# Performance work log

Hardware: AMD Instinct MI355X
Metric: run time of the kernel (lower is better)

## Reference

```python
import jax, jax.numpy as jnp
from jax import lax
import numpy as np

B, N, C, M = 4, 20000, 512, 1024  # batch, points, seed_feat_dim, M_POINT
GRASPNESS_THRESHOLD = 0.1


def setup_inputs() -> dict:
    key = jax.random.key(0)
    k1, k2, k3, k4 = jax.random.split(key, 4)
    return {
        "point_clouds": jax.random.uniform(k1, (B, N, 3), jnp.float32),
        "seed_features": jax.random.normal(k2, (B, C, N), jnp.float32),
        "objectness_score": jax.random.normal(k3, (B, 2, N), jnp.float32),
        "graspness_score": jax.random.normal(k4, (B, N), jnp.float32),
    }


def _fps(xyz, mask, m):
    """Furthest point sampling restricted to masked-valid points.
    xyz: (n,3), mask: (n,) bool. Returns (m,) int indices.
    Matches compacted-array FPS: first pick = first valid point."""
    n = xyz.shape[0]
    first = jnp.argmax(mask)
    mind0 = jnp.full((n,), jnp.inf, xyz.dtype)

    def step(carry, _):
        mind, last = carry
        d = jnp.sum((xyz - xyz[last]) ** 2, axis=-1)
        mind = jnp.minimum(mind, d)
        nxt = jnp.argmax(jnp.where(mask, mind, -jnp.inf))
        return (mind, nxt), last

    _, idx = lax.scan(step, (mind0, first), None, length=m)
    return idx


def reference(point_clouds, seed_features, objectness_score, graspness_score):
    # graspable mask: objectness argmax == 1 AND graspness > threshold
    obj_mask = jnp.argmax(objectness_score, axis=1) == 1            # (B,N)
    grasp_mask = graspness_score > GRASPNESS_THRESHOLD              # (B,N)
    mask = obj_mask & grasp_mask

    # masked FPS per batch element (original loops over B)
    fps_idx = jax.vmap(_fps, in_axes=(0, 0, None))(point_clouds, mask, M)  # (B,M)
    xyz_g = jnp.take_along_axis(point_clouds, fps_idx[:, :, None], axis=1)  # (B,M,3)

    # three_nn: 3 nearest neighbors of each sampled point in the full cloud
    d2 = jnp.sum((xyz_g[:, :, None, :] - point_clouds[:, None, :, :]) ** 2, axis=-1)  # (B,M,N)
    neg_d2, idx3 = lax.top_k(-d2, 3)                                # (B,M,3)
    dist = jnp.sqrt(jnp.maximum(-neg_d2, 0.0))
    w = 1.0 / (dist + 1e-8)
    w = w / jnp.sum(w, axis=-1, keepdims=True)                      # (B,M,3)

    # three_interpolate: inverse-distance-weighted gather of features
    feats_n = seed_features.transpose(0, 2, 1)                      # (B,N,C)
    nb = jax.vmap(lambda f, i: f[i])(feats_n, idx3)                 # (B,M,3,C)
    interp = jnp.einsum("bmkc,bmk->bcm", nb, w)                   # (B,C,M)
    return interp
```

## Files before the change

### kernel.cpp

```cpp
#include <hip/hip_runtime.h>
#include <cstdint>

#define BB 4
#define NN 20000
#define CC 512
#define MM 1024
#define GTHR 0.1f
#define FPS_T 512
#define LDSCAP 5120
#define QB 8

#define INFF __builtin_huge_valf()

__global__ __launch_bounds__(1024) void compact_kernel(
    const float* __restrict__ pc, const float* __restrict__ obj,
    const float* __restrict__ grasp, float4* __restrict__ cxyz,
    int* __restrict__ nv) {
  const int b = blockIdx.x;
  const int t = threadIdx.x;
  const int lane = t & 63, w = t >> 6;
  __shared__ int wtot[16];
  const float* pcb = pc + (size_t)b * NN * 3;
  const float* o0 = obj + (size_t)b * 2 * NN;
  const float* o1 = o0 + NN;
  const float* gb = grasp + (size_t)b * NN;
  float4* cxyzb = cxyz + (size_t)b * NN;

  const int SPAN = 1250;
  const int wstart = w * SPAN;

  unsigned vmask = 0;
  int cnt = 0;
#pragma unroll
  for (int g = 0; g < 20; ++g) {
    int off = g * 64 + lane;
    bool v = false;
    if (off < SPAN) {
      int i = wstart + off;
      float a0 = o0[i], a1 = o1[i], gg = gb[i];
      v = (a1 > a0) && (gg > GTHR);
    }
    unsigned long long bal = __ballot(v);
    if (v) vmask |= (1u << g);
    cnt += (int)__popcll(bal);
  }
  if (lane == 0) wtot[w] = cnt;
  __syncthreads();
  int base = 0;
#pragma unroll
  for (int k = 0; k < 16; ++k)
    if (k < w) base += wtot[k];
#pragma unroll
  for (int g = 0; g < 20; ++g) {
    int off = g * 64 + lane;
    bool v = (vmask >> g) & 1u;
    unsigned long long bal = __ballot(v);
    if (v) {
      int i = wstart + off;
      int pos = base + (int)__popcll(bal & ((1ull << lane) - 1ull));
      cxyzb[pos] = make_float4(pcb[3 * i], pcb[3 * i + 1], pcb[3 * i + 2], 0.f);
    }
    base += (int)__popcll(bal);
  }
  if (t == 0) {
    int tot = 0;
#pragma unroll
    for (int k = 0; k < 16; ++k) tot += wtot[k];
    nv[b] = tot;
  }
}

template <int K>
__device__ void fps_lds(int nv_, const float4* __restrict__ cxyzb,
                        float4* __restrict__ fpsXyzb,
                        float* lx, float* ly, float* lz,
                        unsigned long long (*pk)[8]) {
  const int t = threadIdx.x;
  const int lane = t & 63, w = t >> 6;
  float x[K], y[K], z[K], mind[K];
#pragma unroll
  for (int s = 0; s < K; ++s) {
    int j = s * FPS_T + t;
    if (j < nv_) {
      float4 p = cxyzb[j];
      x[s] = p.x; y[s] = p.y; z[s] = p.z; mind[s] = INFF;
      lx[j] = p.x; ly[j] = p.y; lz[j] = p.z;
    } else {
      x[s] = 0.f; y[s] = 0.f; z[s] = 0.f; mind[s] = 0.f;
    }
  }
  __syncthreads();
  float qx = lx[0], qy = ly[0], qz = lz[0];
  if (t == 0) fpsXyzb[0] = make_float4(qx, qy, qz, 0.f);
  int buf = 0;
  for (int r = 1; r < MM; ++r) {
    float bm = -1.f;
    int bs = 0;
#pragma unroll
    for (int s = 0; s < K; ++s) {
      float dx = x[s] - qx, dy = y[s] - qy, dz = z[s] - qz;
      float d = fmaf(dz, dz, fmaf(dy, dy, dx * dx));
      float m = fminf(mind[s], d);
      mind[s] = m;
      bool better = m > bm;
      bm = better ? m : bm;
      bs = better ? s : bs;
    }
    unsigned j = (unsigned)(bs * FPS_T + t);
    unsigned long long key =
        ((unsigned long long)__float_as_uint(bm) << 32) | (unsigned)(~j);
#pragma unroll
    for (int off = 32; off; off >>= 1) {
      unsigned long long ok = __shfl_xor(key, off);
      key = ok > key ? ok : key;
    }
    if (lane == 0) pk[buf][w] = key;
    __syncthreads();
    unsigned long long k0 = pk[buf][lane & 7];
    unsigned long long k1 = __shfl_xor(k0, 1); k0 = k1 > k0 ? k1 : k0;
    k1 = __shfl_xor(k0, 2); k0 = k1 > k0 ? k1 : k0;
    k1 = __shfl_xor(k0, 4); k0 = k1 > k0 ? k1 : k0;
    unsigned jw = ~(unsigned)(k0 & 0xffffffffull);
    qx = lx[jw]; qy = ly[jw]; qz = lz[jw];
    if (t == 0) fpsXyzb[r] = make_float4(qx, qy, qz, 0.f);
    buf ^= 1;
  }
}

__device__ void fps_fallback(int nv_, const float4* __restrict__ cxyzb,
                             float4* __restrict__ fpsXyzb,
                             float* __restrict__ mindg,
                             unsigned long long (*pk)[8]) {
  const int t = threadIdx.x;
  const int lane = t & 63, w = t >> 6;
  for (int j = t; j < nv_; j += FPS_T) mindg[j] = INFF;
  __syncthreads();
  float4 q = cxyzb[0];
  float qx = q.x, qy = q.y, qz = q.z;
  if (t == 0) fpsXyzb[0] = make_float4(qx, qy, qz, 0.f);
  int buf = 0;
  for (int r = 1; r < MM; ++r) {
    float bm = -1.f;
    int bj = 0x7fffffff;
    for (int j = t; j < nv_; j += FPS_T) {
      float4 p = cxyzb[j];
      float dx = p.x - qx, dy = p.y - qy, dz = p.z - qz;
      float d = fmaf(dz, dz, fmaf(dy, dy, dx * dx));
      float m = fminf(mindg[j], d);
      mindg[j] = m;
      bool better = m > bm;
      bm = better ? m : bm;
      bj = better ? j : bj;
    }
    unsigned long long key =
        ((unsigned long long)__float_as_uint(bm) << 32) | (unsigned)(~bj);
#pragma unroll
    for (int off = 32; off; off >>= 1) {
      unsigned long long ok = __shfl_xor(key, off);
      key = ok > key ? ok : key;
    }
    if (lane == 0) pk[buf][w] = key;
    __syncthreads();
    unsigned long long k0 = pk[buf][lane & 7];
    unsigned long long k1 = __shfl_xor(k0, 1); k0 = k1 > k0 ? k1 : k0;
    k1 = __shfl_xor(k0, 2); k0 = k1 > k0 ? k1 : k0;
    k1 = __shfl_xor(k0, 4); k0 = k1 > k0 ? k1 : k0;
    unsigned jw = ~(unsigned)(k0 & 0xffffffffull);
    float4 qq = cxyzb[jw];
    qx = qq.x; qy = qq.y; qz = qq.z;
    if (t == 0) fpsXyzb[r] = make_float4(qx, qy, qz, 0.f);
    buf ^= 1;
  }
}

__global__ __launch_bounds__(FPS_T) void fps_kernel(
    const float* __restrict__ pc, const float4* __restrict__ cxyz,
    const int* __restrict__ nv, float4* __restrict__ fpsXyz,
    float* __restrict__ mindg) {
  __shared__ float lx[LDSCAP], ly[LDSCAP], lz[LDSCAP];
  __shared__ unsigned long long pk[2][8];
  int b = blockIdx.x;
  int nv_ = nv[b];
  const float4* cxyzb = cxyz + (size_t)b * NN;
  float4* fpsXyzb = fpsXyz + (size_t)b * MM;
  if (nv_ == 0) {
    int t = threadIdx.x;
    const float* pcb = pc + (size_t)b * NN * 3;
    float4 p0 = make_float4(pcb[0], pcb[1], pcb[2], 0.f);
    for (int r = t; r < MM; r += FPS_T) fpsXyzb[r] = p0;
    return;
  }
  int slots = (nv_ + FPS_T - 1) / FPS_T;
  if (slots <= 3)       fps_lds<3>(nv_, cxyzb, fpsXyzb, lx, ly, lz, pk);
  else if (slots <= 6)  fps_lds<6>(nv_, cxyzb, fpsXyzb, lx, ly, lz, pk);
  else if (slots <= 9)  fps_lds<9>(nv_, cxyzb, fpsXyzb, lx, ly, lz, pk);
  else if (slots <= 10) fps_lds<10>(nv_, cxyzb, fpsXyzb, lx, ly, lz, pk);
  else fps_fallback(nv_, cxyzb, fpsXyzb, mindg + (size_t)b * NN, pk);
}

__device__ __forceinline__ bool nn_before(float ad, int ai, float bd, int bi) {
  return (ad < bd) || (ad == bd && ai < bi);
}

__device__ __forceinline__ void merge3(float* ad, int* ai,
                                       float b0, float b1, float b2,
                                       int j0, int j1, int j2) {
  bool c0 = nn_before(ad[0], ai[0], b0, j0);
  float r0d = c0 ? ad[0] : b0; int r0i = c0 ? ai[0] : j0;
  float Xd = c0 ? b0 : ad[0];  int Xi = c0 ? j0 : ai[0];
  bool c1 = nn_before(ad[1], ai[1], b1, j1);
  float Yd = c1 ? ad[1] : b1;  int Yi = c1 ? ai[1] : j1;
  bool c2 = nn_before(Xd, Xi, Yd, Yi);
  float r1d = c2 ? Xd : Yd;    int r1i = c2 ? Xi : Yi;
  float Wd = c2 ? Yd : Xd;     int Wi = c2 ? Yi : Xi;
  bool c3 = nn_before(ad[2], ai[2], b2, j2);
  float Vd = c3 ? ad[2] : b2;  int Vi = c3 ? ai[2] : j2;
  bool c4 = nn_before(Wd, Wi, Vd, Vi);
  float r2d = c4 ? Wd : Vd;    int r2i = c4 ? Wi : Vi;
  ad[0] = r0d; ad[1] = r1d; ad[2] = r2d;
  ai[0] = r0i; ai[1] = r1i; ai[2] = r2i;
}

__global__ void three_nn_kernel(const float* __restrict__ pc,
                                const float4* __restrict__ fpsXyz,
                                int* __restrict__ idx3,
                                float* __restrict__ w3) {
  const int blk = blockIdx.x;
  const int b = blk / (MM / QB);
  const int qbase = (blk % (MM / QB)) * QB;
  const int t = threadIdx.x;
  const int lane = t & 63, w = t >> 6;
  const float* pcb = pc + (size_t)b * NN * 3;
  float qx[QB], qy[QB], qz[QB];
#pragma unroll
  for (int qq = 0; qq < QB; ++qq) {
    float4 p = fpsXyz[(size_t)b * MM + qbase + qq];
    qx[qq] = p.x; qy[qq] = p.y; qz[qq] = p.z;
  }
  float qd[QB][3]; int qi[QB][3];
#pragma unroll
  for (int qq = 0; qq < QB; ++qq)
#pragma unroll
    for (int k = 0; k < 3; ++k) { qd[qq][k] = INFF; qi[qq][k] = 0x7fffffff; }

  const int nchunk = (NN + 255) / 256;
  for (int c = 0; c < nchunk; ++c) {
    int i = c * 256 + t;
    if (i < NN) {
      float pxx = pcb[3 * i], pyy = pcb[3 * i + 1], pzz = pcb[3 * i + 2];
#pragma unroll
      for (int qq = 0; qq < QB; ++qq) {
        float dx = pxx - qx[qq], dy = pyy - qy[qq], dz = pzz - qz[qq];
        float d = fmaf(dz, dz, fmaf(dy, dy, dx * dx));
        if (d < qd[qq][2]) {
          bool lt0 = d < qd[qq][0], lt1 = d < qd[qq][1];
          qd[qq][2] = lt1 ? qd[qq][1] : d;  qi[qq][2] = lt1 ? qi[qq][1] : i;
          float nd1 = lt0 ? qd[qq][0] : (lt1 ? d : qd[qq][1]);
          int   ni1 = lt0 ? qi[qq][0] : (lt1 ? i : qi[qq][1]);
          qd[qq][1] = nd1; qi[qq][1] = ni1;
          qd[qq][0] = lt0 ? d : qd[qq][0];  qi[qq][0] = lt0 ? i : qi[qq][0];
        }
      }
    }
  }
#pragma unroll
  for (int off = 32; off; off >>= 1) {
#pragma unroll
    for (int qq = 0; qq < QB; ++qq) {
      float bd0 = __shfl_xor(qd[qq][0], off);
      float bd1 = __shfl_xor(qd[qq][1], off);
      float bd2 = __shfl_xor(qd[qq][2], off);
      int bi0 = __shfl_xor(qi[qq][0], off);
      int bi1 = __shfl_xor(qi[qq][1], off);
      int bi2 = __shfl_xor(qi[qq][2], off);
      merge3(qd[qq], qi[qq], bd0, bd1, bd2, bi0, bi1, bi2);
    }
  }
  __shared__ float smd[4][QB][3];
  __shared__ int smi[4][QB][3];
  if (lane == 0) {
#pragma unroll
    for (int qq = 0; qq < QB; ++qq)
#pragma unroll
      for (int k = 0; k < 3; ++k) { smd[w][qq][k] = qd[qq][k]; smi[w][qq][k] = qi[qq][k]; }
  }
  __syncthreads();
  if (t < QB) {
    int qq = t;
    float fd[3]; int fi[3];
#pragma unroll
    for (int k = 0; k < 3; ++k) { fd[k] = smd[0][qq][k]; fi[k] = smi[0][qq][k]; }
#pragma unroll
    for (int ww = 1; ww < 4; ++ww)
      merge3(fd, fi, smd[ww][qq][0], smd[ww][qq][1], smd[ww][qq][2],
             smi[ww][qq][0], smi[ww][qq][1], smi[ww][qq][2]);
    float wa = 1.f / (sqrtf(fmaxf(fd[0], 0.f)) + 1e-8f);
    float wb = 1.f / (sqrtf(fmaxf(fd[1], 0.f)) + 1e-8f);
    float wc = 1.f / (sqrtf(fmaxf(fd[2], 0.f)) + 1e-8f);
    float s = wa + wb + wc;
    size_t base3 = ((size_t)b * MM + qbase + qq) * 3;
    w3[base3] = wa / s; w3[base3 + 1] = wb / s; w3[base3 + 2] = wc / s;
    idx3[base3] = fi[0]; idx3[base3 + 1] = fi[1]; idx3[base3 + 2] = fi[2];
  }
}

__global__ void interp_kernel(const float* __restrict__ seed,
                              const int* __restrict__ idx3,
                              const float* __restrict__ w3,
                              float* __restrict__ out) {
  const int blk = blockIdx.x;
  const int b = blk / CC;
  const int c = blk % CC;
  const float* row = seed + ((size_t)b * CC + c) * NN;
  const int t = threadIdx.x;
#pragma unroll
  for (int u = 0; u < MM / 256; ++u) {
    int m = u * 256 + t;
    size_t base3 = ((size_t)b * MM + m) * 3;
    int i0 = idx3[base3], i1 = idx3[base3 + 1], i2 = idx3[base3 + 2];
    float w0 = w3[base3], w1 = w3[base3 + 1], w2 = w3[base3 + 2];
    float v = fmaf(w2, row[i2], fmaf(w1, row[i1], w0 * row[i0]));
    out[((size_t)b * CC + c) * MM + m] = v;
  }
}

extern "C" void kernel_launch(void* const* d_in, const int* in_sizes, int n_in,
                              void* d_out, int out_size, void* d_ws,
                              size_t ws_size, hipStream_t stream) {
  (void)in_sizes; (void)n_in; (void)out_size; (void)ws_size;
  const float* pc = (const float*)d_in[0];
  const float* seed = (const float*)d_in[1];
  const float* obj = (const float*)d_in[2];
  const float* grasp = (const float*)d_in[3];
  float* out = (float*)d_out;

  char* p = (char*)d_ws;
  float4* cxyz = (float4*)p;   p += sizeof(float4) * BB * NN;
  float4* fpsXyz = (float4*)p; p += sizeof(float4) * BB * MM;
  int* idx3 = (int*)p;         p += sizeof(int) * BB * MM * 3;
  float* w3 = (float*)p;       p += sizeof(float) * BB * MM * 3;
  float* mindg = (float*)p;    p += sizeof(float) * BB * NN;
  int* nv = (int*)p;           p += sizeof(int) * BB;

  hipLaunchKernelGGL(compact_kernel, dim3(BB), dim3(1024), 0, stream,
                     pc, obj, grasp, cxyz, nv);
  hipLaunchKernelGGL(fps_kernel, dim3(BB), dim3(FPS_T), 0, stream,
                     pc, cxyz, nv, fpsXyz, mindg);
  hipLaunchKernelGGL(three_nn_kernel, dim3(BB * MM / QB), dim3(256), 0, stream,
                     pc, fpsXyz, idx3, w3);
  hipLaunchKernelGGL(interp_kernel, dim3(BB * CC), dim3(256), 0, stream,
                     seed, idx3, w3, out);
}
```

Measured before the change: 1.133 ms.

## Fuse mask compaction into FPS kernel and use value-only wave max with ballot index

Merges the separate compaction kernel into the FPS kernel: each block computes the graspable mask, prefix-sums per wave, and writes compacted xyz straight into LDS, going through global memory only when the count exceeds LDS capacity. This removes one launch and a global round trip. The per-iteration argmax now reduces only the float distance with DPP/swizzle, then recovers the index with a ballot over matching slots, and the cross-wave merge reads packed keys with vector LDS loads. The tie-breaking and zero-mind padding lanes could change which index is chosen in edge cases.

```diff
diff --git a/kernel.cpp b/kernel.cpp
--- a/kernel.cpp
+++ b/kernel.cpp
@@ -11,70 +11,43 @@
 #define QB 8
 
 #define INFF __builtin_huge_valf()
-
-__global__ __launch_bounds__(1024) void compact_kernel(
-    const float* __restrict__ pc, const float* __restrict__ obj,
-    const float* __restrict__ grasp, float4* __restrict__ cxyz,
-    int* __restrict__ nv) {
-  const int b = blockIdx.x;
-  const int t = threadIdx.x;
-  const int lane = t & 63, w = t >> 6;
-  __shared__ int wtot[16];
-  const float* pcb = pc + (size_t)b * NN * 3;
-  const float* o0 = obj + (size_t)b * 2 * NN;
-  const float* o1 = o0 + NN;
-  const float* gb = grasp + (size_t)b * NN;
-  float4* cxyzb = cxyz + (size_t)b * NN;
-
-  const int SPAN = 1250;
-  const int wstart = w * SPAN;
-
-  unsigned vmask = 0;
-  int cnt = 0;
-#pragma unroll
-  for (int g = 0; g < 20; ++g) {
-    int off = g * 64 + lane;
-    bool v = false;
-    if (off < SPAN) {
-      int i = wstart + off;
-      float a0 = o0[i], a1 = o1[i], gg = gb[i];
-      v = (a1 > a0) && (gg > GTHR);
-    }
-    unsigned long long bal = __ballot(v);
-    if (v) vmask |= (1u << g);
-    cnt += (int)__popcll(bal);
-  }
-  if (lane == 0) wtot[w] = cnt;
-  __syncthreads();
-  int base = 0;
-#pragma unroll
-  for (int k = 0; k < 16; ++k)
-    if (k < w) base += wtot[k];
-#pragma unroll
-  for (int g = 0; g < 20; ++g) {
-    int off = g * 64 + lane;
-    bool v = (vmask >> g) & 1u;
-    unsigned long long bal = __ballot(v);
-    if (v) {
-      int i = wstart + off;
-      int pos = base + (int)__popcll(bal & ((1ull << lane) - 1ull));
-      cxyzb[pos] = make_float4(pcb[3 * i], pcb[3 * i + 1], pcb[3 * i + 2], 0.f);
-    }
-    base += (int)__popcll(bal);
-  }
-  if (t == 0) {
-    int tot = 0;
-#pragma unroll
-    for (int k = 0; k < 16; ++k) tot += wtot[k];
-    nv[b] = tot;
-  }
+typedef unsigned long long u64;
+
+__device__ __forceinline__ float wave_max_f32(float v) {
+  int i = __float_as_int(v);
+  i = __builtin_amdgcn_update_dpp(i, i, 0x121, 0xF, 0xF, false);
+  v = fmaxf(v, __int_as_float(i));
+  i = __float_as_int(v);
+  i = __builtin_amdgcn_update_dpp(i, i, 0x122, 0xF, 0xF, false);
+  v = fmaxf(v, __int_as_float(i));
+  i = __float_as_int(v);
+  i = __builtin_amdgcn_update_dpp(i, i, 0x124, 0xF, 0xF, false);
+  v = fmaxf(v, __int_as_float(i));
+  i = __float_as_int(v);
+  i = __builtin_amdgcn_update_dpp(i, i, 0x128, 0xF, 0xF, false);
+  v = fmaxf(v, __int_as_float(i));
+  v = fmaxf(v, __int_as_float(
+                   __builtin_amdgcn_ds_swizzle(__float_as_int(v), 0x401F)));
+  v = fmaxf(v, __shfl_xor(v, 32));
+  return v;
+}
+
+__device__ __forceinline__ unsigned merge8(const u64* pkrow) {
+  const ulonglong2* p2 = (const ulonglong2*)pkrow;
+  ulonglong2 e0 = p2[0], e1 = p2[1], e2 = p2[2], e3 = p2[3];
+  u64 a = e0.x > e0.y ? e0.x : e0.y;
+  u64 b = e1.x > e1.y ? e1.x : e1.y;
+  u64 c = e2.x > e2.y ? e2.x : e2.y;
+  u64 d = e3.x > e3.y ? e3.x : e3.y;
+  a = a > b ? a : b;
+  c = c > d ? c : d;
+  a = a > c ? a : c;
+  return ~(unsigned)(a & 0xffffffffull);
 }
 
 template <int K>
-__device__ void fps_lds(int nv_, const float4* __restrict__ cxyzb,
-                        float4* __restrict__ fpsXyzb,
-                        float* lx, float* ly, float* lz,
-                        unsigned long long (*pk)[8]) {
+__device__ void fps_lds(int nv_, const float2* lxy, const float* lz,
+                        float4* fpsXyzb, u64 (*pk)[8]) {
   const int t = threadIdx.x;
   const int lane = t & 63, w = t >> 6;
   float x[K], y[K], z[K], mind[K];
@@ -82,91 +55,89 @@
   for (int s = 0; s < K; ++s) {
     int j = s * FPS_T + t;
     if (j < nv_) {
-      float4 p = cxyzb[j];
-      x[s] = p.x; y[s] = p.y; z[s] = p.z; mind[s] = INFF;
-      lx[j] = p.x; ly[j] = p.y; lz[j] = p.z;
+      float2 p = lxy[j];
+      x[s] = p.x; y[s] = p.y; z[s] = lz[j]; mind[s] = INFF;
     } else {
       x[s] = 0.f; y[s] = 0.f; z[s] = 0.f; mind[s] = 0.f;
     }
   }
-  __syncthreads();
-  float qx = lx[0], qy = ly[0], qz = lz[0];
+  float2 q0 = lxy[0];
+  float qx = q0.x, qy = q0.y, qz = lz[0];
   if (t == 0) fpsXyzb[0] = make_float4(qx, qy, qz, 0.f);
   int buf = 0;
   for (int r = 1; r < MM; ++r) {
-    float bm = -1.f;
-    int bs = 0;
+    float bm;
 #pragma unroll
     for (int s = 0; s < K; ++s) {
       float dx = x[s] - qx, dy = y[s] - qy, dz = z[s] - qz;
       float d = fmaf(dz, dz, fmaf(dy, dy, dx * dx));
       float m = fminf(mind[s], d);
       mind[s] = m;
-      bool better = m > bm;
-      bm = better ? m : bm;
-      bs = better ? s : bs;
-    }
-    unsigned j = (unsigned)(bs * FPS_T + t);
-    unsigned long long key =
-        ((unsigned long long)__float_as_uint(bm) << 32) | (unsigned)(~j);
-#pragma unroll
-    for (int off = 32; off; off >>= 1) {
-      unsigned long long ok = __shfl_xor(key, off);
-      key = ok > key ? ok : key;
-    }
-    if (lane == 0) pk[buf][w] = key;
+      bm = (s == 0) ? m : fmaxf(bm, m);
+    }
+    bm = wave_max_f32(bm);
+    unsigned jw = 0u;
+    bool found = false;
+#pragma unroll
+    for (int s = 0; s < K; ++s) {
+      if (!found) {
+        u64 bal = __ballot(mind[s] == bm);
+        if (bal) {
+          jw = (unsigned)(s * FPS_T + (w << 6)) +
+               (unsigned)__builtin_ctzll(bal);
+          found = true;
+        }
+      }
+    }
+    if (lane == 0)
+      pk[buf][w] = ((u64)__float_as_uint(bm) << 32) | (unsigned)~jw;
     __syncthreads();
-    unsigned long long k0 = pk[buf][lane & 7];
-    unsigned long long k1 = __shfl_xor(k0, 1); k0 = k1 > k0 ? k1 : k0;
-    k1 = __shfl_xor(k0, 2); k0 = k1 > k0 ? k1 : k0;
-    k1 = __shfl_xor(k0, 4); k0 = k1 > k0 ? k1 : k0;
-    unsigned jw = ~(unsigned)(k0 & 0xffffffffull);
-    qx = lx[jw]; qy = ly[jw]; qz = lz[jw];
+    unsigned jg = merge8(&pk[buf][0]);
+    float2 qq = lxy[jg];
+    qx = qq.x; qy = qq.y; qz = lz[jg];
     if (t == 0) fpsXyzb[r] = make_float4(qx, qy, qz, 0.f);
     buf ^= 1;
   }
 }
 
-__device__ void fps_fallback(int nv_, const float4* __restrict__ cxyzb,
-                             float4* __restrict__ fpsXyzb,
-                             float* __restrict__ mindg,
-                             unsigned long long (*pk)[8]) {
+__device__ void fps_fallback(int nv_, const float4* cxg, float4* fpsXyzb,
+                             float* mindg, u64 (*pk)[8]) {
   const int t = threadIdx.x;
   const int lane = t & 63, w = t >> 6;
   for (int j = t; j < nv_; j += FPS_T) mindg[j] = INFF;
   __syncthreads();
-  float4 q = cxyzb[0];
+  float4 q = cxg[0];
   float qx = q.x, qy = q.y, qz = q.z;
   if (t == 0) fpsXyzb[0] = make_float4(qx, qy, qz, 0.f);
   int buf = 0;
+  const int kmax = (nv_ + FPS_T - 1) / FPS_T;
   for (int r = 1; r < MM; ++r) {
-    float bm = -1.f;
-    int bj = 0x7fffffff;
+    float bm = 0.f;
     for (int j = t; j < nv_; j += FPS_T) {
-      float4 p = cxyzb[j];
+      float4 p = cxg[j];
       float dx = p.x - qx, dy = p.y - qy, dz = p.z - qz;
       float d = fmaf(dz, dz, fmaf(dy, dy, dx * dx));
       float m = fminf(mindg[j], d);
       mindg[j] = m;
-      bool better = m > bm;
-      bm = better ? m : bm;
-      bj = better ? j : bj;
-    }
-    unsigned long long key =
-        ((unsigned long long)__float_as_uint(bm) << 32) | (unsigned)(~bj);
-#pragma unroll
-    for (int off = 32; off; off >>= 1) {
-      unsigned long long ok = __shfl_xor(key, off);
-      key = ok > key ? ok : key;
-    }
-    if (lane == 0) pk[buf][w] = key;
+      bm = fmaxf(bm, m);
+    }
+    bm = wave_max_f32(bm);
+    unsigned jw = 0u;
+    bool found = false;
+    for (int k = 0; k < kmax && !found; ++k) {
+      int j = k * FPS_T + t;
+      bool match = (j < nv_) && (mindg[j] == bm);
+      u64 bal = __ballot(match);
+      if (bal) {
+        jw = (unsigned)(k * FPS_T + (w << 6)) + (unsigned)__builtin_ctzll(bal);
+        found = true;
+      }
+    }
+    if (lane == 0)
+      pk[buf][w] = ((u64)__float_as_uint(bm) << 32) | (unsigned)~jw;
     __syncthreads();
-    unsigned long long k0 = pk[buf][lane & 7];
-    unsigned long long k1 = __shfl_xor(k0, 1); k0 = k1 > k0 ? k1 : k0;
-    k1 = __shfl_xor(k0, 2); k0 = k1 > k0 ? k1 : k0;
-    k1 = __shfl_xor(k0, 4); k0 = k1 > k0 ? k1 : k0;
-    unsigned jw = ~(unsigned)(k0 & 0xffffffffull);
-    float4 qq = cxyzb[jw];
+    unsigned jg = merge8(&pk[buf][0]);
+    float4 qq = cxg[jg];
     qx = qq.x; qy = qq.y; qz = qq.z;
     if (t == 0) fpsXyzb[r] = make_float4(qx, qy, qz, 0.f);
     buf ^= 1;
@@ -174,28 +145,75 @@
 }
 
 __global__ __launch_bounds__(FPS_T) void fps_kernel(
-    const float* __restrict__ pc, const float4* __restrict__ cxyz,
-    const int* __restrict__ nv, float4* __restrict__ fpsXyz,
-    float* __restrict__ mindg) {
-  __shared__ float lx[LDSCAP], ly[LDSCAP], lz[LDSCAP];
-  __shared__ unsigned long long pk[2][8];
-  int b = blockIdx.x;
-  int nv_ = nv[b];
-  const float4* cxyzb = cxyz + (size_t)b * NN;
+    const float* __restrict__ pc, const float* __restrict__ obj,
+    const float* __restrict__ grasp, float4* __restrict__ fpsXyz,
+    float4* __restrict__ cxyz_g, float* __restrict__ mindg) {
+  __shared__ float2 lxy[LDSCAP];
+  __shared__ float lz[LDSCAP];
+  __shared__ alignas(16) u64 pk[2][8];
+  __shared__ int wtot[8];
+  const int b = blockIdx.x;
+  const int t = threadIdx.x;
+  const int lane = t & 63, w = t >> 6;
+  const float* pcb = pc + (size_t)b * NN * 3;
+  const float* o0 = obj + (size_t)b * 2 * NN;
+  const float* o1 = o0 + NN;
+  const float* gb = grasp + (size_t)b * NN;
   float4* fpsXyzb = fpsXyz + (size_t)b * MM;
+  float4* cxg = cxyz_g + (size_t)b * NN;
+
+  const int SPAN = 2500;
+  const int wstart = w * SPAN;
+  u64 vmask = 0;
+  int cnt = 0;
+#pragma unroll
+  for (int g = 0; g < 40; ++g) {
+    int off = g * 64 + lane;
+    bool v = false;
+    if (off < SPAN) {
+      int i = wstart + off;
+      v = (o1[i] > o0[i]) && (gb[i] > GTHR);
+    }
+    u64 bal = __ballot(v);
+    if (v) vmask |= (1ull << g);
+    cnt += (int)__popcll(bal);
+  }
+  if (lane == 0) wtot[w] = cnt;
+  __syncthreads();
+  int base = 0, nv_ = 0;
+#pragma unroll
+  for (int k = 0; k < 8; ++k) {
+    int c = wtot[k];
+    if (k < w) base += c;
+    nv_ += c;
+  }
+  const bool useg = (nv_ > LDSCAP);
+#pragma unroll
+  for (int g = 0; g < 40; ++g) {
+    bool v = (vmask >> g) & 1ull;
+    u64 bal = __ballot(v);
+    if (v) {
+      int i = wstart + g * 64 + lane;
+      float xx = pcb[3 * i], yy = pcb[3 * i + 1], zz = pcb[3 * i + 2];
+      int pos = base + (int)__popcll(bal & ((1ull << lane) - 1ull));
+      if (pos < LDSCAP) { lxy[pos] = make_float2(xx, yy); lz[pos] = zz; }
+      if (useg) cxg[pos] = make_float4(xx, yy, zz, 0.f);
+    }
+    base += (int)__popcll(bal);
+  }
+  __syncthreads();
+
   if (nv_ == 0) {
-    int t = threadIdx.x;
-    const float* pcb = pc + (size_t)b * NN * 3;
     float4 p0 = make_float4(pcb[0], pcb[1], pcb[2], 0.f);
     for (int r = t; r < MM; r += FPS_T) fpsXyzb[r] = p0;
     return;
   }
   int slots = (nv_ + FPS_T - 1) / FPS_T;
-  if (slots <= 3)       fps_lds<3>(nv_, cxyzb, fpsXyzb, lx, ly, lz, pk);
-  else if (slots <= 6)  fps_lds<6>(nv_, cxyzb, fpsXyzb, lx, ly, lz, pk);
-  else if (slots <= 9)  fps_lds<9>(nv_, cxyzb, fpsXyzb, lx, ly, lz, pk);
-  else if (slots <= 10) fps_lds<10>(nv_, cxyzb, fpsXyzb, lx, ly, lz, pk);
-  else fps_fallback(nv_, cxyzb, fpsXyzb, mindg + (size_t)b * NN, pk);
+  if (slots <= 3)       fps_lds<3>(nv_, lxy, lz, fpsXyzb, pk);
+  else if (slots <= 6)  fps_lds<6>(nv_, lxy, lz, fpsXyzb, pk);
+  else if (slots <= 9)  fps_lds<9>(nv_, lxy, lz, fpsXyzb, pk);
+  else if (slots <= 10) fps_lds<10>(nv_, lxy, lz, fpsXyzb, pk);
+  else fps_fallback(nv_, cxg, fpsXyzb, mindg + (size_t)b * NN, pk);
 }
 
 __device__ __forceinline__ bool nn_before(float ad, int ai, float bd, int bi) {
@@ -340,12 +358,9 @@
   int* idx3 = (int*)p;         p += sizeof(int) * BB * MM * 3;
   float* w3 = (float*)p;       p += sizeof(float) * BB * MM * 3;
   float* mindg = (float*)p;    p += sizeof(float) * BB * NN;
-  int* nv = (int*)p;           p += sizeof(int) * BB;
-
-  hipLaunchKernelGGL(compact_kernel, dim3(BB), dim3(1024), 0, stream,
-                     pc, obj, grasp, cxyz, nv);
+
   hipLaunchKernelGGL(fps_kernel, dim3(BB), dim3(FPS_T), 0, stream,
-                     pc, cxyz, nv, fpsXyz, mindg);
+                     pc, obj, grasp, fpsXyz, cxyz, mindg);
   hipLaunchKernelGGL(three_nn_kernel, dim3(BB * MM / QB), dim3(256), 0, stream,
                      pc, fpsXyz, idx3, w3);
   hipLaunchKernelGGL(interp_kernel, dim3(BB * CC), dim3(256), 0, stream,
```

New measurement: 1.262 ms. 11.5% more time.
